# Kernel tuning notes

Hardware: AMD Instinct MI355X
Metric: run time of the kernel (lower is better)

## Reference

```python
import jax, jax.numpy as jnp
import numpy as np

D_MODEL = 256
N_LAYERS = 4
D_STATE = 16
D_CONV = 4
EXPAND = 2
HEADDIM = 64
D_INNER = EXPAND * D_MODEL            # 512
NHEADS = D_INNER // HEADDIM           # 8
CONV_DIM = D_INNER + 2 * D_STATE      # 544 (ngroups=1)
D_IN_PROJ = 2 * D_INNER + 2 * D_STATE + NHEADS  # 1064
VOCAB = 8
MAXLEN = 2048
NCLASSES = 2
PAD_IDX = 4
EPS = 1e-5
B, L = 8, 2048


def setup_inputs() -> dict:
    key = jax.random.key(0)
    ks = jax.random.split(key, 10)
    x = jax.random.randint(ks[0], (B, L), 0, VOCAB)
    attention_mask = jnp.ones((B, L), jnp.float32)
    embedding = 0.02 * jax.random.normal(ks[1], (VOCAB, D_MODEL), jnp.float32)
    embedding = embedding.at[PAD_IDX].set(0.0)  # padding_idx row is zero
    pos_embedding = 0.02 * jax.random.normal(ks[2], (1, MAXLEN, D_MODEL), jnp.float32)
    in_proj_w = 0.05 * jax.random.normal(ks[3], (N_LAYERS, D_IN_PROJ, D_MODEL), jnp.float32)
    conv_w = 0.3 * jax.random.normal(ks[4], (N_LAYERS, CONV_DIM, D_CONV), jnp.float32)
    conv_b = jnp.zeros((N_LAYERS, CONV_DIM), jnp.float32)
    # dt_bias = softplus^{-1}(dt) with dt ~ U(0.001, 0.1), as in mamba_ssm init
    dt = jax.random.uniform(ks[5], (N_LAYERS, NHEADS), jnp.float32, 0.001, 0.1)
    dt_bias = jnp.log(jnp.expm1(dt))
    A_log = jnp.log(jax.random.uniform(ks[6], (N_LAYERS, NHEADS), jnp.float32, 1.0, 16.0))
    D_param = jnp.ones((N_LAYERS, NHEADS), jnp.float32)
    norm_w = jnp.ones((N_LAYERS, D_INNER), jnp.float32)
    out_proj_w = 0.05 * jax.random.normal(ks[7], (N_LAYERS, D_MODEL, D_INNER), jnp.float32)
    ln_w = jnp.ones((D_MODEL,), jnp.float32)
    ln_b = jnp.zeros((D_MODEL,), jnp.float32)
    cls_w = 0.05 * jax.random.normal(ks[8], (NCLASSES, D_MODEL), jnp.float32)
    cls_b = jnp.zeros((NCLASSES,), jnp.float32)
    return dict(x=x, attention_mask=attention_mask, embedding=embedding,
                pos_embedding=pos_embedding, in_proj_w=in_proj_w, conv_w=conv_w,
                conv_b=conv_b, dt_bias=dt_bias, A_log=A_log, D_param=D_param,
                norm_w=norm_w, out_proj_w=out_proj_w, ln_w=ln_w, ln_b=ln_b,
                cls_w=cls_w, cls_b=cls_b)


def _mamba2(h_in, Wi, cw, cb, dtb, Alog, Dp, nw, Wo):
    """One Mamba2 block (ngroups=1, headdim=64, norm_before_gate=False)."""
    b, l, _ = h_in.shape
    zxbcdt = jnp.einsum('bld,ed->ble', h_in, Wi)          # (b,l,1064)
    z = zxbcdt[..., :D_INNER]                             # gate
    xBC = zxbcdt[..., D_INNER:D_INNER + CONV_DIM]
    dt = jax.nn.softplus(zxbcdt[..., D_INNER + CONV_DIM:] + dtb)  # (b,l,h)
    # causal depthwise conv1d (kernel D_CONV) + silu
    xp = jnp.pad(xBC, ((0, 0), (D_CONV - 1, 0), (0, 0)))
    xwin = jnp.stack([xp[:, k:k + l, :] for k in range(D_CONV)], axis=-1)  # (b,l,c,k)
    xBC = jax.nn.silu(jnp.einsum('blck,ck->blc', xwin, cw) + cb)
    xs = xBC[..., :D_INNER].reshape(b, l, NHEADS, HEADDIM)
    Bm = xBC[..., D_INNER:D_INNER + D_STATE]              # (b,l,n)
    Cm = xBC[..., D_INNER + D_STATE:]                     # (b,l,n)
    dA = jnp.exp(dt * (-jnp.exp(Alog)))                   # (b,l,h)
    dtx = dt[..., None] * xs                              # (b,l,h,p)

    def step(h, inp):
        dA_t, dtx_t, B_t, C_t = inp
        h = dA_t[:, :, None, None] * h + dtx_t[..., None] * B_t[:, None, None, :]
        y = jnp.einsum('bhpn,bn->bhp', h, C_t)
        return h, y

    h0 = jnp.zeros((b, NHEADS, HEADDIM, D_STATE), h_in.dtype)
    _, ys = jax.lax.scan(step, h0, (jnp.swapaxes(dA, 0, 1), jnp.swapaxes(dtx, 0, 1),
                                    jnp.swapaxes(Bm, 0, 1), jnp.swapaxes(Cm, 0, 1)))
    y = jnp.swapaxes(ys, 0, 1) + Dp[None, None, :, None] * xs  # skip term D*x
    y = y.reshape(b, l, D_INNER) * jax.nn.silu(z)               # gate, then RMSNorm
    y = y * jax.lax.rsqrt(jnp.mean(jnp.square(y), axis=-1, keepdims=True) + EPS) * nw
    return jnp.einsum('ble,de->bld', y, Wo)


def _layer_norm(h, w, b):
    mu = jnp.mean(h, -1, keepdims=True)
    var = jnp.mean(jnp.square(h - mu), -1, keepdims=True)
    return (h - mu) * jax.lax.rsqrt(var + EPS) * w + b


def reference(x, attention_mask, embedding, pos_embedding, in_proj_w, conv_w,
              conv_b, dt_bias, A_log, D_param, norm_w, out_proj_w, ln_w, ln_b,
              cls_w, cls_b):
    l = x.shape[1]
    h = embedding[x] + pos_embedding[:, :l, :]
    m = attention_mask[..., None]
    h = h * m
    for i in range(N_LAYERS):
        res = h
        h = _mamba2(h, in_proj_w[i], conv_w[i], conv_b[i], dt_bias[i],
                    A_log[i], D_param[i], norm_w[i], out_proj_w[i])
        h = _layer_norm(h + res, ln_w, ln_b)
        h = h * m
    pooled = jnp.mean(h, axis=1)   # dropout is identity at eval
    return pooled @ cls_w.T + cls_b
```

## Files before the change

### kernel.cpp

```cpp
#include <hip/hip_runtime.h>
#include <hip/hip_bf16.h>
#include <math.h>

#define B_ 8
#define L_ 2048
#define DM 256
#define DIP 1064
#define DI 512
#define CD 544
#define DSZ 16
#define NH 8
#define HD 64
#define Q_ 64
#define NC 32

typedef __attribute__((ext_vector_type(8))) short bf16x8;
typedef __attribute__((ext_vector_type(4))) float f32x4;

__device__ inline unsigned short f2bf(float f) {
    __hip_bfloat16 h = __float2bfloat16(f);
    return *(unsigned short*)&h;
}
__device__ inline float bf2f(unsigned short u) {
    unsigned int x = ((unsigned int)u) << 16;
    return __uint_as_float(x);
}
__device__ inline float fast_sig(float x) {
    return __builtin_amdgcn_rcpf(1.f + __expf(-x));
}

__global__ __launch_bounds__(256) void k_f2bf(const float* __restrict__ in, unsigned short* __restrict__ out, int n4) {
    int i = blockIdx.x * 256 + threadIdx.x;
    if (i >= n4) return;
    float4 v = *(const float4*)(in + (size_t)i * 4);
    ushort4 o;
    o.x = f2bf(v.x); o.y = f2bf(v.y); o.z = f2bf(v.z); o.w = f2bf(v.w);
    *(ushort4*)(out + (size_t)i * 4) = o;
}

__global__ __launch_bounds__(256) void k_embed(const int* __restrict__ x, const float* __restrict__ mask,
                                               const float* __restrict__ emb, const float* __restrict__ pos,
                                               float* __restrict__ h, unsigned short* __restrict__ h_bf) {
    int i = blockIdx.x * 256 + threadIdx.x;
    if (i >= B_ * L_ * DM) return;
    int d = i % DM;
    int bl = i / DM;
    int l = bl % L_;
    int tok = x[bl];
    float v = (emb[tok * DM + d] + pos[l * DM + d]) * mask[bl];
    h[i] = v;
    h_bf[i] = f2bf(v);
}

template <int OUTMODE>
__global__ __launch_bounds__(256) void k_gemm(const unsigned short* __restrict__ A, int lda,
                                              const unsigned short* __restrict__ Bw, int ldb, int N,
                                              void* __restrict__ Cout, int ldc, int K,
                                              float* __restrict__ dtraw) {
    __shared__ unsigned short Al[2][128 * 32];
    __shared__ unsigned short Bl[2][128 * 32];
    int tid = threadIdx.x;
    int l = tid & 63;
    int w = tid >> 6, wr = w >> 1, wc = w & 1;
    int m0 = blockIdx.x * 128, n0 = blockIdx.y * 128;

    f32x4 zero = {0.f, 0.f, 0.f, 0.f};
    f32x4 acc[4][4];
#pragma unroll
    for (int i = 0; i < 4; i++)
#pragma unroll
        for (int j = 0; j < 4; j++) acc[i][j] = zero;

    int lr = l & 15, kq = l >> 4;
    int aoff = (wr * 64 + lr) * 32 + kq * 8;
    int boff = (wc * 64 + lr) * 32 + kq * 8;

    auto stage = [&](int ks, int buf) {
        int k0 = ks * 32;
#pragma unroll
        for (int q = 0; q < 2; q++) {
            int c = tid + q * 256;
            int row = c >> 2, cc = (c & 3) * 8;
            const unsigned short* ga = A + (size_t)(m0 + row) * lda + k0 + cc;
            __builtin_amdgcn_global_load_lds((const __attribute__((address_space(1))) void*)ga,
                                             (__attribute__((address_space(3))) void*)(&Al[buf][c * 8]), 16, 0, 0);
            int rowb = n0 + row;
            if (rowb > N - 1) rowb = N - 1;
            const unsigned short* gb = Bw + (size_t)rowb * ldb + k0 + cc;
            __builtin_amdgcn_global_load_lds((const __attribute__((address_space(1))) void*)gb,
                                             (__attribute__((address_space(3))) void*)(&Bl[buf][c * 8]), 16, 0, 0);
        }
    };

    stage(0, 0);
    int ksteps = K / 32;
    for (int s = 0; s < ksteps; s++) {
        int buf = s & 1;
        __syncthreads();
        if (s + 1 < ksteps) stage(s + 1, buf ^ 1);
        bf16x8 a[4], b[4];
#pragma unroll
        for (int i = 0; i < 4; i++) a[i] = *(const bf16x8*)&Al[buf][aoff + i * 512];
#pragma unroll
        for (int j = 0; j < 4; j++) b[j] = *(const bf16x8*)&Bl[buf][boff + j * 512];
#pragma unroll
        for (int i = 0; i < 4; i++)
#pragma unroll
            for (int j = 0; j < 4; j++)
                acc[i][j] = __builtin_amdgcn_mfma_f32_16x16x32_bf16(a[i], b[j], acc[i][j], 0, 0, 0);
    }

#pragma unroll
    for (int i = 0; i < 4; i++) {
        int m = m0 + wr * 64 + i * 16 + kq * 4;
#pragma unroll
        for (int j = 0; j < 4; j++) {
            int n = n0 + wc * 64 + j * 16 + lr;
            if (n < N) {
                if (OUTMODE == 0) {
                    float* C = (float*)Cout;
#pragma unroll
                    for (int r = 0; r < 4; r++)
                        C[(size_t)(m + r) * ldc + n] = acc[i][j][r];
                } else {
                    unsigned short* C = (unsigned short*)Cout;
#pragma unroll
                    for (int r = 0; r < 4; r++)
                        C[(size_t)(m + r) * ldc + n] = f2bf(acc[i][j][r]);
                    if (OUTMODE == 1 && n >= DI + CD) {
#pragma unroll
                        for (int r = 0; r < 4; r++)
                            dtraw[(size_t)(m + r) * NH + (n - (DI + CD))] = acc[i][j][r];
                    }
                }
            }
        }
    }
}

__global__ __launch_bounds__(256) void k_scan1c(const unsigned short* __restrict__ zxb,
                                                const float* __restrict__ dtraw,
                                                const float* __restrict__ cw, const float* __restrict__ cb,
                                                const float* __restrict__ dtb, const float* __restrict__ Alog,
                                                const float* __restrict__ Dp,
                                                unsigned short* __restrict__ ybuf, float* __restrict__ Sg,
                                                float* __restrict__ Pg, float* __restrict__ cumLg,
                                                float* __restrict__ Cc) {
    int bh = blockIdx.x, c = blockIdx.y;
    int b = bh >> 3, h = bh & 7;
    int tid = threadIdx.x;
    int t0 = c * Q_;
    int w = tid >> 6, l = tid & 63;
    int lr = l & 15, kq = l >> 4;

    __shared__ __align__(16) unsigned short Zl[67 * 96];
    __shared__ __align__(16) unsigned short Xt[Q_ * 72];
    __shared__ __align__(16) unsigned short Cbf[Q_ * 32];
    __shared__ __align__(16) unsigned short Bbf[Q_ * 32];
    __shared__ __align__(16) unsigned short Btw[DSZ * 72];
    __shared__ float Lc[Q_], dts[Q_], coefS[Q_];
    unsigned short* Mbf = Zl;

    float Dval = Dp[h];

    for (int idx = tid; idx < 67 * 12; idx += 256) {
        int rr = idx / 12, seg = idx - rr * 12;
        int lg = t0 - 3 + rr;
        bf16x8 v;
        if (lg >= 0) {
            const unsigned short* src = zxb + (size_t)(b * L_ + lg) * DIP +
                                        (seg < 8 ? (DI + h * HD + seg * 8) : (1024 + (seg - 8) * 8));
            v = *(const bf16x8*)src;
        } else {
#pragma unroll
            for (int j = 0; j < 8; j++) v[j] = 0;
        }
        int col = (seg < 8) ? seg * 8 : (64 + (seg - 8) * 8);
        *(bf16x8*)&Zl[rr * 96 + col] = v;
    }
    {
        bf16x8 z8;
#pragma unroll
        for (int j = 0; j < 8; j++) z8[j] = 0;
        *(bf16x8*)&Cbf[tid * 8] = z8;
        *(bf16x8*)&Bbf[tid * 8] = z8;
    }
    if (tid < 64) {
        float raw = dtraw[(size_t)(b * L_ + t0 + tid) * NH + h] + dtb[h];
        float dtv = (raw > 20.f) ? raw : log1pf(__expf(raw));
        float v = -__expf(Alog[h]) * dtv;
#pragma unroll
        for (int off = 1; off < 64; off <<= 1) {
            float u = __shfl_up(v, off);
            if (tid >= off) v += u;
        }
        dts[tid] = dtv;
        Lc[tid] = v;
        float lend = __shfl(v, 63);
        coefS[tid] = __expf(lend - v) * dtv;
        cumLg[(size_t)(bh * NC + c) * Q_ + tid] = v;
        if (tid == 63) Pg[bh * NC + c] = __expf(v);
    }
    __syncthreads();

    float xreg[4][4];
#pragma unroll
    for (int pt = 0; pt < 4; pt++) {
#pragma unroll
        for (int r = 0; r < 4; r++) {
            int t = w * 16 + kq * 4 + r;
            int p = pt * 16 + lr;
            int cc = h * HD + p;
            float acc = cb[cc];
#pragma unroll
            for (int k = 0; k < 4; k++)
                acc = fmaf(bf2f(Zl[(t + k) * 96 + p]), cw[cc * 4 + k], acc);
            float s = acc * fast_sig(acc);
            xreg[pt][r] = s;
            Xt[p * 72 + t] = f2bf(s);
        }
    }
    for (int idx = tid; idx < Q_ * 32; idx += 256) {
        int t = idx >> 5, n32 = idx & 31;
        int cc = DI + n32;
        float acc = cb[cc];
#pragma unroll
        for (int k = 0; k < 4; k++)
            acc = fmaf(bf2f(Zl[(t + k) * 96 + 64 + n32]), cw[cc * 4 + k], acc);
        float s = acc * fast_sig(acc);
        if (n32 < 16) {
            int n = n32;
            Bbf[t * 32 + (((n >> 3) ^ (t & 3)) * 8) + (n & 7)] = f2bf(dts[t] * s);
            Btw[n * 72 + t] = f2bf(coefS[t] * s);
        } else {
            int n = n32 - 16;
            Cbf[t * 32 + (((n >> 3) ^ (t & 3)) * 8) + (n & 7)] = f2bf(s);
            if (h == 0) Cc[((size_t)(b * L_ + t0 + t)) * DSZ + n] = s;
        }
    }
    __syncthreads();

    f32x4 zero = {0.f, 0.f, 0.f, 0.f};

    f32x4 cbt[4];
    {
        bf16x8 af = *(const bf16x8*)&Cbf[(w * 16 + lr) * 32 + ((kq ^ (lr & 3)) * 8)];
#pragma unroll
        for (int st = 0; st < 4; st++) {
            bf16x8 bf = *(const bf16x8*)&Bbf[(st * 16 + lr) * 32 + ((kq ^ (lr & 3)) * 8)];
            cbt[st] = __builtin_amdgcn_mfma_f32_16x16x32_bf16(af, bf, zero, 0, 0, 0);
        }
    }
#pragma unroll
    for (int st = 0; st < 4; st++) {
#pragma unroll
        for (int r = 0; r < 4; r++) {
            int t = w * 16 + kq * 4 + r;
            int s = st * 16 + lr;
            float m = (s <= t) ? __expf(Lc[t] - Lc[s]) * cbt[st][r] : 0.f;
            Mbf[t * 64 + (((s >> 3) ^ (t & 7)) * 8) + (s & 7)] = f2bf(m);
        }
    }
    __syncthreads();

    {
        unsigned short* base_y = ybuf + ((size_t)b * L_ + t0) * DI + h * HD;
        f32x4 acc[4];
#pragma unroll
        for (int pt = 0; pt < 4; pt++) acc[pt] = zero;
#pragma unroll
        for (int ks = 0; ks < 2; ks++) {
            bf16x8 af = *(const bf16x8*)&Mbf[(w * 16 + lr) * 64 + (((ks * 4 + kq) ^ (lr & 7)) * 8)];
#pragma unroll
            for (int pt = 0; pt < 4; pt++) {
                bf16x8 bf = *(const bf16x8*)&Xt[(pt * 16 + lr) * 72 + ks * 32 + kq * 8];
                acc[pt] = __builtin_amdgcn_mfma_f32_16x16x32_bf16(af, bf, acc[pt], 0, 0, 0);
            }
        }
#pragma unroll
        for (int pt = 0; pt < 4; pt++) {
#pragma unroll
            for (int r = 0; r < 4; r++) {
                int t = w * 16 + kq * 4 + r;
                int p = pt * 16 + lr;
                base_y[(size_t)t * DI + p] = f2bf(acc[pt][r] + Dval * xreg[pt][r]);
            }
        }
    }

    {
        f32x4 sacc = zero;
#pragma unroll
        for (int ks = 0; ks < 2; ks++) {
            bf16x8 af = *(const bf16x8*)&Xt[(w * 16 + lr) * 72 + ks * 32 + kq * 8];
            bf16x8 bf = *(const bf16x8*)&Btw[lr * 72 + ks * 32 + kq * 8];
            sacc = __builtin_amdgcn_mfma_f32_16x16x32_bf16(af, bf, sacc, 0, 0, 0);
        }
#pragma unroll
        for (int r = 0; r < 4; r++) {
            int p = w * 16 + kq * 4 + r;
            Sg[((size_t)(bh * NC + c) * HD + p) * DSZ + lr] = sacc[r];
        }
    }
}

__global__ __launch_bounds__(256) void k_scan2(const float* __restrict__ Sg, const float* __restrict__ Pg,
                                               float* __restrict__ Hg) {
    int bh = blockIdx.x;
    int tid = threadIdx.x;
    int p = tid >> 2, n0 = (tid & 3) * 4;
    float4 H = make_float4(0.f, 0.f, 0.f, 0.f);
    for (int g = 0; g < NC / 8; g++) {
        float4 S[8];
#pragma unroll
        for (int j = 0; j < 8; j++)
            S[j] = *(const float4*)(Sg + (((size_t)bh * NC + g * 8 + j) * HD + p) * DSZ + n0);
#pragma unroll
        for (int j = 0; j < 8; j++) {
            int cc = g * 8 + j;
            *(float4*)(Hg + (((size_t)bh * NC + cc) * HD + p) * DSZ + n0) = H;
            float P = Pg[bh * NC + cc];
            H.x = fmaf(P, H.x, S[j].x);
            H.y = fmaf(P, H.y, S[j].y);
            H.z = fmaf(P, H.z, S[j].z);
            H.w = fmaf(P, H.w, S[j].w);
        }
    }
}

__global__ __launch_bounds__(256) void k_scan3g(const unsigned short* __restrict__ ybuf,
                                                const unsigned short* __restrict__ zxb,
                                                const float* __restrict__ Hg, const float* __restrict__ cumLg,
                                                const float* __restrict__ Cc, const float* __restrict__ nw,
                                                unsigned short* __restrict__ yn_bf) {
    int b = blockIdx.x, by = blockIdx.y;
    int c64 = by >> 2, tl0 = (by & 3) * 16;
    int t0 = by * 16;
    int tid = threadIdx.x;
    __shared__ float Hsn[DSZ * 576];
    __shared__ float Lq[NH][16];

    {
        int p = tid & 63, hp = tid >> 6;
#pragma unroll
        for (int ho = 0; ho < 2; ho++) {
            int hh = hp * 2 + ho;
            const float* src = Hg + (((size_t)(b * NH + hh) * NC + c64) * HD + p) * DSZ;
            float* dst = &Hsn[p * 9 + hh];
#pragma unroll
            for (int nq = 0; nq < 4; nq++) {
                float4 v = *(const float4*)(src + nq * 4);
                dst[(nq * 4 + 0) * 576] = v.x;
                dst[(nq * 4 + 1) * 576] = v.y;
                dst[(nq * 4 + 2) * 576] = v.z;
                dst[(nq * 4 + 3) * 576] = v.w;
            }
        }
    }
    if (tid < 128) {
        int hh = tid >> 4, t = tid & 15;
        Lq[hh][t] = cumLg[((size_t)(b * NH + hh) * NC + c64) * Q_ + tl0 + t];
    }
    __syncthreads();

    int t = tid >> 4, q = tid & 15;
    int hh = q >> 1, p0 = (q & 1) * 32;
    size_t bl = (size_t)b * L_ + t0 + t;
    float ef = __expf(Lq[hh][t]);

    float Cr[16];
#pragma unroll
    for (int k = 0; k < 4; k++) {
        float4 v = *(const float4*)(Cc + bl * DSZ + k * 4);
        Cr[4 * k + 0] = ef * v.x;
        Cr[4 * k + 1] = ef * v.y;
        Cr[4 * k + 2] = ef * v.z;
        Cr[4 * k + 3] = ef * v.w;
    }

    const unsigned short* yrow = ybuf + bl * DI + hh * HD + p0;
    const unsigned short* zrow = zxb + bl * DIP + hh * HD + p0;
    unsigned short yv[32], zv[32];
#pragma unroll
    for (int k = 0; k < 4; k++) *(bf16x8*)&yv[k * 8] = *(const bf16x8*)(yrow + k * 8);
#pragma unroll
    for (int k = 0; k < 4; k++) *(bf16x8*)&zv[k * 8] = *(const bf16x8*)(zrow + k * 8);

    float yg[32];
    float ss = 0.f;
#pragma unroll
    for (int j = 0; j < 32; j++) {
        const float* hp_ = &Hsn[(p0 + j) * 9 + hh];
        float d = 0.f;
#pragma unroll
        for (int n = 0; n < DSZ; n++) d = fmaf(Cr[n], hp_[n * 576], d);
        float y = bf2f(yv[j]) + d;
        float z = bf2f(zv[j]);
        yg[j] = y * z * fast_sig(z);
        ss = fmaf(yg[j], yg[j], ss);
    }
    ss += __shfl_xor(ss, 1);
    ss += __shfl_xor(ss, 2);
    ss += __shfl_xor(ss, 4);
    ss += __shfl_xor(ss, 8);
    float r = rsqrtf(ss * (1.f / DI) + 1e-5f);

    const float* nwp = nw + hh * HD + p0;
    unsigned short* dst = yn_bf + bl * DI + hh * HD + p0;
#pragma unroll
    for (int k = 0; k < 4; k++) {
        bf16x8 o;
#pragma unroll
        for (int j = 0; j < 8; j++) o[j] = (short)f2bf(yg[k * 8 + j] * r * nwp[k * 8 + j]);
        *(bf16x8*)(dst + k * 8) = o;
    }
}

__global__ __launch_bounds__(256) void k_ln(const unsigned short* __restrict__ tmp, float* __restrict__ h,
                                            unsigned short* __restrict__ h_bf,
                                            const float* __restrict__ lnw, const float* __restrict__ lnb,
                                            const float* __restrict__ mask) {
    int row = blockIdx.x * 4 + (threadIdx.x >> 6);
    int lane = threadIdx.x & 63;
    size_t base = (size_t)row * DM + lane * 4;
    ushort4 tv = *(const ushort4*)(tmp + base);
    float4 hv = *(const float4*)(h + base);
    float v[4] = {bf2f(tv.x) + hv.x, bf2f(tv.y) + hv.y, bf2f(tv.z) + hv.z, bf2f(tv.w) + hv.w};
    float s = v[0] + v[1] + v[2] + v[3];
#pragma unroll
    for (int m = 1; m < 64; m <<= 1) s += __shfl_xor(s, m);
    float mu = s * (1.f / DM);
    float q = 0.f;
#pragma unroll
    for (int j = 0; j < 4; j++) {
        float d = v[j] - mu;
        q = fmaf(d, d, q);
    }
#pragma unroll
    for (int m = 1; m < 64; m <<= 1) q += __shfl_xor(q, m);
    float rs = rsqrtf(q * (1.f / DM) + 1e-5f);
    float mk = mask[row];
    float4 wv = *(const float4*)(lnw + lane * 4);
    float4 bv = *(const float4*)(lnb + lane * 4);
    float o[4];
    o[0] = ((v[0] - mu) * rs * wv.x + bv.x) * mk;
    o[1] = ((v[1] - mu) * rs * wv.y + bv.y) * mk;
    o[2] = ((v[2] - mu) * rs * wv.z + bv.z) * mk;
    o[3] = ((v[3] - mu) * rs * wv.w + bv.w) * mk;
    *(float4*)(h + base) = make_float4(o[0], o[1], o[2], o[3]);
    ushort4 ob;
    ob.x = f2bf(o[0]); ob.y = f2bf(o[1]); ob.z = f2bf(o[2]); ob.w = f2bf(o[3]);
    *(ushort4*)(h_bf + base) = ob;
}

__global__ __launch_bounds__(256) void k_pool1(const float* __restrict__ h, float* __restrict__ part) {
    int b = blockIdx.x, g = blockIdx.y, d = threadIdx.x;
    const float* hb = h + ((size_t)b * L_ + g * 128) * DM + d;
    float s = 0.f;
    for (int l = 0; l < 128; l++) s += hb[(size_t)l * DM];
    part[((size_t)b * 16 + g) * DM + d] = s;
}

__global__ __launch_bounds__(256) void k_pool2(const float* __restrict__ part, const float* __restrict__ cw,
                                               const float* __restrict__ cb, float* __restrict__ out) {
    int b = blockIdx.x, tid = threadIdx.x;
    float s = 0.f;
#pragma unroll
    for (int g = 0; g < 16; g++) s += part[((size_t)b * 16 + g) * DM + tid];
    s *= (1.0f / L_);
    float p0 = s * cw[tid];
    float p1 = s * cw[DM + tid];
#pragma unroll
    for (int m = 1; m < 64; m <<= 1) {
        p0 += __shfl_xor(p0, m);
        p1 += __shfl_xor(p1, m);
    }
    __shared__ float r0[4], r1[4];
    if ((tid & 63) == 0) { r0[tid >> 6] = p0; r1[tid >> 6] = p1; }
    __syncthreads();
    if (tid == 0) {
        out[b * 2 + 0] = r0[0] + r0[1] + r0[2] + r0[3] + cb[0];
        out[b * 2 + 1] = r1[0] + r1[1] + r1[2] + r1[3] + cb[1];
    }
}

extern "C" void kernel_launch(void* const* d_in, const int* in_sizes, int n_in,
                              void* d_out, int out_size, void* d_ws, size_t ws_size,
                              hipStream_t stream) {
    const int*   x    = (const int*)d_in[0];
    const float* mask = (const float*)d_in[1];
    const float* emb  = (const float*)d_in[2];
    const float* pos  = (const float*)d_in[3];
    const float* Wi   = (const float*)d_in[4];
    const float* cw   = (const float*)d_in[5];
    const float* cb   = (const float*)d_in[6];
    const float* dtb  = (const float*)d_in[7];
    const float* Alog = (const float*)d_in[8];
    const float* Dp   = (const float*)d_in[9];
    const float* nw   = (const float*)d_in[10];
    const float* Wo   = (const float*)d_in[11];
    const float* lnw  = (const float*)d_in[12];
    const float* lnb  = (const float*)d_in[13];
    const float* clsw = (const float*)d_in[14];
    const float* clsb = (const float*)d_in[15];
    float* out = (float*)d_out;

    float* ws    = (float*)d_ws;
    float* h     = ws;
    float* dtraw = h + (size_t)B_ * L_ * DM;
    float* Sg    = dtraw + (size_t)B_ * L_ * NH;
    float* Pg    = Sg + (size_t)64 * NC * HD * DSZ;
    float* cumL  = Pg + (size_t)64 * NC;
    float* Hg    = cumL + (size_t)64 * NC * Q_;
    float* Cc    = Hg + (size_t)64 * NC * HD * DSZ;
    float* pool  = Cc + (size_t)B_ * L_ * DSZ;
    unsigned short* zxb   = (unsigned short*)(pool + (size_t)B_ * 16 * DM);
    unsigned short* ybuf  = zxb + (size_t)B_ * L_ * DIP;
    unsigned short* tmp   = ybuf + (size_t)B_ * L_ * DI;
    unsigned short* h_bf  = tmp + (size_t)B_ * L_ * DM;
    unsigned short* yn_bf = h_bf + (size_t)B_ * L_ * DM;
    unsigned short* Wi_bf = yn_bf + (size_t)B_ * L_ * DI;
    unsigned short* Wo_bf = Wi_bf + (size_t)4 * DIP * DM;

    k_f2bf<<<(4 * DIP * DM / 4 + 255) / 256, 256, 0, stream>>>(Wi, Wi_bf, 4 * DIP * DM / 4);
    k_f2bf<<<(4 * DM * DI / 4 + 255) / 256, 256, 0, stream>>>(Wo, Wo_bf, 4 * DM * DI / 4);

    k_embed<<<(B_ * L_ * DM + 255) / 256, 256, 0, stream>>>(x, mask, emb, pos, h, h_bf);

    for (int i = 0; i < 4; i++) {
        k_gemm<1><<<dim3(B_ * L_ / 128, (DIP + 127) / 128), 256, 0, stream>>>(
            h_bf, DM, Wi_bf + (size_t)i * DIP * DM, DM, DIP, zxb, DIP, DM, dtraw);
        k_scan1c<<<dim3(64, NC), 256, 0, stream>>>(
            zxb, dtraw, cw + (size_t)i * CD * 4, cb + i * CD, dtb + i * NH, Alog + i * NH,
            Dp + i * NH, ybuf, Sg, Pg, cumL, Cc);
        k_scan2<<<64, 256, 0, stream>>>(Sg, Pg, Hg);
        k_scan3g<<<dim3(B_, 128), 256, 0, stream>>>(ybuf, zxb, Hg, cumL, Cc, nw + (size_t)i * DI, yn_bf);
        k_gemm<2><<<dim3(B_ * L_ / 128, DM / 128), 256, 0, stream>>>(
            yn_bf, DI, Wo_bf + (size_t)i * DM * DI, DI, DM, tmp, DM, DI, nullptr);
        k_ln<<<B_ * L_ / 4, 256, 0, stream>>>(tmp, h, h_bf, lnw, lnb, mask);
    }

    k_pool1<<<dim3(B_, 16), 256, 0, stream>>>(h, pool);
    k_pool2<<<B_, 256, 0, stream>>>(pool, clsw, clsb, out);
}
```

Baseline: 416.7 us.

## Fuse out-projection GEMM with residual add and LayerNorm, drop fp32 hidden state

Replaces the out-projection GEMM plus separate LayerNorm kernel with a single kernel that computes 32-row by 256-column tiles, adds the residual read from the bf16 hidden state, and does the row LayerNorm in-register with cross-wave reductions through shared memory. The fp32 hidden-state buffer and the intermediate tmp buffer are removed, and pooling now reads bf16. This cuts a kernel launch and several full-tensor round trips through memory. In exchange the residual stream is held only in bf16, which loses precision across layers, and variance is computed as E[x^2]-mu^2 in a single pass.

```diff
diff --git a/kernel.cpp b/kernel.cpp
--- a/kernel.cpp
+++ b/kernel.cpp
@@ -40,7 +40,7 @@
 
 __global__ __launch_bounds__(256) void k_embed(const int* __restrict__ x, const float* __restrict__ mask,
                                                const float* __restrict__ emb, const float* __restrict__ pos,
-                                               float* __restrict__ h, unsigned short* __restrict__ h_bf) {
+                                               unsigned short* __restrict__ h_bf) {
     int i = blockIdx.x * 256 + threadIdx.x;
     if (i >= B_ * L_ * DM) return;
     int d = i % DM;
@@ -48,7 +48,6 @@
     int l = bl % L_;
     int tok = x[bl];
     float v = (emb[tok * DM + d] + pos[l * DM + d]) * mask[bl];
-    h[i] = v;
     h_bf[i] = f2bf(v);
 }
 
@@ -117,22 +116,130 @@
         for (int j = 0; j < 4; j++) {
             int n = n0 + wc * 64 + j * 16 + lr;
             if (n < N) {
-                if (OUTMODE == 0) {
-                    float* C = (float*)Cout;
+                unsigned short* C = (unsigned short*)Cout;
+#pragma unroll
+                for (int r = 0; r < 4; r++)
+                    C[(size_t)(m + r) * ldc + n] = f2bf(acc[i][j][r]);
+                if (OUTMODE == 1 && n >= DI + CD) {
 #pragma unroll
                     for (int r = 0; r < 4; r++)
-                        C[(size_t)(m + r) * ldc + n] = acc[i][j][r];
-                } else {
-                    unsigned short* C = (unsigned short*)Cout;
-#pragma unroll
-                    for (int r = 0; r < 4; r++)
-                        C[(size_t)(m + r) * ldc + n] = f2bf(acc[i][j][r]);
-                    if (OUTMODE == 1 && n >= DI + CD) {
-#pragma unroll
-                        for (int r = 0; r < 4; r++)
-                            dtraw[(size_t)(m + r) * NH + (n - (DI + CD))] = acc[i][j][r];
-                    }
+                        dtraw[(size_t)(m + r) * NH + (n - (DI + CD))] = acc[i][j][r];
                 }
+            }
+        }
+    }
+}
+
+__global__ __launch_bounds__(256) void k_gemm_ln(const unsigned short* __restrict__ A,
+                                                 const unsigned short* __restrict__ Bw,
+                                                 unsigned short* __restrict__ hbf,
+                                                 const float* __restrict__ lnw, const float* __restrict__ lnb,
+                                                 const float* __restrict__ mask) {
+    __shared__ unsigned short Al[2][32 * 32];
+    __shared__ unsigned short Bl[2][256 * 32];
+    __shared__ float part_s[32][4], part_q[32][4];
+    int tid = threadIdx.x;
+    int l = tid & 63;
+    int w = tid >> 6;
+    int m0 = blockIdx.x * 32;
+    int lr = l & 15, kq = l >> 4;
+
+    f32x4 zero = {0.f, 0.f, 0.f, 0.f};
+    f32x4 acc[2][4];
+#pragma unroll
+    for (int i = 0; i < 2; i++)
+#pragma unroll
+        for (int j = 0; j < 4; j++) acc[i][j] = zero;
+
+    auto stage = [&](int ks, int buf) {
+        int k0 = ks * 32;
+        if (tid < 128) {
+            int row = tid >> 2, cc = (tid & 3) * 8;
+            const unsigned short* ga = A + (size_t)(m0 + row) * DI + k0 + cc;
+            __builtin_amdgcn_global_load_lds((const __attribute__((address_space(1))) void*)ga,
+                                             (__attribute__((address_space(3))) void*)(&Al[buf][tid * 8]), 16, 0, 0);
+        }
+#pragma unroll
+        for (int q = 0; q < 4; q++) {
+            int c = tid + q * 256;
+            int row = c >> 2, cc = (c & 3) * 8;
+            const unsigned short* gb = Bw + (size_t)row * DI + k0 + cc;
+            __builtin_amdgcn_global_load_lds((const __attribute__((address_space(1))) void*)gb,
+                                             (__attribute__((address_space(3))) void*)(&Bl[buf][c * 8]), 16, 0, 0);
+        }
+    };
+
+    stage(0, 0);
+    const int ksteps = DI / 32;
+    for (int s = 0; s < ksteps; s++) {
+        int buf = s & 1;
+        __syncthreads();
+        if (s + 1 < ksteps) stage(s + 1, buf ^ 1);
+        bf16x8 a[2], b[4];
+#pragma unroll
+        for (int i = 0; i < 2; i++) a[i] = *(const bf16x8*)&Al[buf][(i * 16 + lr) * 32 + kq * 8];
+#pragma unroll
+        for (int j = 0; j < 4; j++) b[j] = *(const bf16x8*)&Bl[buf][(w * 64 + j * 16 + lr) * 32 + kq * 8];
+#pragma unroll
+        for (int i = 0; i < 2; i++)
+#pragma unroll
+            for (int j = 0; j < 4; j++)
+                acc[i][j] = __builtin_amdgcn_mfma_f32_16x16x32_bf16(a[i], b[j], acc[i][j], 0, 0, 0);
+    }
+
+#pragma unroll
+    for (int i = 0; i < 2; i++) {
+#pragma unroll
+        for (int r = 0; r < 4; r++) {
+            int row = i * 16 + kq * 4 + r;
+            const unsigned short* hrow = hbf + (size_t)(m0 + row) * DM + w * 64 + lr;
+#pragma unroll
+            for (int j = 0; j < 4; j++)
+                acc[i][j][r] += bf2f(hrow[j * 16]);
+        }
+    }
+#pragma unroll
+    for (int i = 0; i < 2; i++) {
+#pragma unroll
+        for (int r = 0; r < 4; r++) {
+            float sv = acc[i][0][r] + acc[i][1][r] + acc[i][2][r] + acc[i][3][r];
+            float qv = acc[i][0][r] * acc[i][0][r] + acc[i][1][r] * acc[i][1][r] +
+                       acc[i][2][r] * acc[i][2][r] + acc[i][3][r] * acc[i][3][r];
+#pragma unroll
+            for (int off = 1; off < 16; off <<= 1) {
+                sv += __shfl_xor(sv, off);
+                qv += __shfl_xor(qv, off);
+            }
+            if (lr == 0) {
+                int row = i * 16 + kq * 4 + r;
+                part_s[row][w] = sv;
+                part_q[row][w] = qv;
+            }
+        }
+    }
+    __syncthreads();
+    float4 wv4 = make_float4(lnw[w * 64 + 0 * 16 + lr], lnw[w * 64 + 1 * 16 + lr],
+                             lnw[w * 64 + 2 * 16 + lr], lnw[w * 64 + 3 * 16 + lr]);
+    float4 bv4 = make_float4(lnb[w * 64 + 0 * 16 + lr], lnb[w * 64 + 1 * 16 + lr],
+                             lnb[w * 64 + 2 * 16 + lr], lnb[w * 64 + 3 * 16 + lr]);
+#pragma unroll
+    for (int i = 0; i < 2; i++) {
+#pragma unroll
+        for (int r = 0; r < 4; r++) {
+            int row = i * 16 + kq * 4 + r;
+            float sum = part_s[row][0] + part_s[row][1] + part_s[row][2] + part_s[row][3];
+            float sq  = part_q[row][0] + part_q[row][1] + part_q[row][2] + part_q[row][3];
+            float mu = sum * (1.f / DM);
+            float var = sq * (1.f / DM) - mu * mu;
+            float rs = rsqrtf(var + 1e-5f);
+            float mk = mask[m0 + row];
+            unsigned short* drow = hbf + (size_t)(m0 + row) * DM + w * 64 + lr;
+            float wr_[4] = {wv4.x, wv4.y, wv4.z, wv4.w};
+            float br_[4] = {bv4.x, bv4.y, bv4.z, bv4.w};
+#pragma unroll
+            for (int j = 0; j < 4; j++) {
+                float o = ((acc[i][j][r] - mu) * rs * wr_[j] + br_[j]) * mk;
+                drow[j * 16] = f2bf(o);
             }
         }
     }
@@ -416,48 +523,11 @@
     }
 }
 
-__global__ __launch_bounds__(256) void k_ln(const unsigned short* __restrict__ tmp, float* __restrict__ h,
-                                            unsigned short* __restrict__ h_bf,
-                                            const float* __restrict__ lnw, const float* __restrict__ lnb,
-                                            const float* __restrict__ mask) {
-    int row = blockIdx.x * 4 + (threadIdx.x >> 6);
-    int lane = threadIdx.x & 63;
-    size_t base = (size_t)row * DM + lane * 4;
-    ushort4 tv = *(const ushort4*)(tmp + base);
-    float4 hv = *(const float4*)(h + base);
-    float v[4] = {bf2f(tv.x) + hv.x, bf2f(tv.y) + hv.y, bf2f(tv.z) + hv.z, bf2f(tv.w) + hv.w};
-    float s = v[0] + v[1] + v[2] + v[3];
-#pragma unroll
-    for (int m = 1; m < 64; m <<= 1) s += __shfl_xor(s, m);
-    float mu = s * (1.f / DM);
-    float q = 0.f;
-#pragma unroll
-    for (int j = 0; j < 4; j++) {
-        float d = v[j] - mu;
-        q = fmaf(d, d, q);
-    }
-#pragma unroll
-    for (int m = 1; m < 64; m <<= 1) q += __shfl_xor(q, m);
-    float rs = rsqrtf(q * (1.f / DM) + 1e-5f);
-    float mk = mask[row];
-    float4 wv = *(const float4*)(lnw + lane * 4);
-    float4 bv = *(const float4*)(lnb + lane * 4);
-    float o[4];
-    o[0] = ((v[0] - mu) * rs * wv.x + bv.x) * mk;
-    o[1] = ((v[1] - mu) * rs * wv.y + bv.y) * mk;
-    o[2] = ((v[2] - mu) * rs * wv.z + bv.z) * mk;
-    o[3] = ((v[3] - mu) * rs * wv.w + bv.w) * mk;
-    *(float4*)(h + base) = make_float4(o[0], o[1], o[2], o[3]);
-    ushort4 ob;
-    ob.x = f2bf(o[0]); ob.y = f2bf(o[1]); ob.z = f2bf(o[2]); ob.w = f2bf(o[3]);
-    *(ushort4*)(h_bf + base) = ob;
-}
-
-__global__ __launch_bounds__(256) void k_pool1(const float* __restrict__ h, float* __restrict__ part) {
+__global__ __launch_bounds__(256) void k_pool1(const unsigned short* __restrict__ h, float* __restrict__ part) {
     int b = blockIdx.x, g = blockIdx.y, d = threadIdx.x;
-    const float* hb = h + ((size_t)b * L_ + g * 128) * DM + d;
+    const unsigned short* hb = h + ((size_t)b * L_ + g * 128) * DM + d;
     float s = 0.f;
-    for (int l = 0; l < 128; l++) s += hb[(size_t)l * DM];
+    for (int l = 0; l < 128; l++) s += bf2f(hb[(size_t)l * DM]);
     part[((size_t)b * 16 + g) * DM + d] = s;
 }
 
@@ -506,8 +576,7 @@
     float* out = (float*)d_out;
 
     float* ws    = (float*)d_ws;
-    float* h     = ws;
-    float* dtraw = h + (size_t)B_ * L_ * DM;
+    float* dtraw = ws;
     float* Sg    = dtraw + (size_t)B_ * L_ * NH;
     float* Pg    = Sg + (size_t)64 * NC * HD * DSZ;
     float* cumL  = Pg + (size_t)64 * NC;
@@ -516,8 +585,7 @@
     float* pool  = Cc + (size_t)B_ * L_ * DSZ;
     unsigned short* zxb   = (unsigned short*)(pool + (size_t)B_ * 16 * DM);
     unsigned short* ybuf  = zxb + (size_t)B_ * L_ * DIP;
-    unsigned short* tmp   = ybuf + (size_t)B_ * L_ * DI;
-    unsigned short* h_bf  = tmp + (size_t)B_ * L_ * DM;
+    unsigned short* h_bf  = ybuf + (size_t)B_ * L_ * DI;
     unsigned short* yn_bf = h_bf + (size_t)B_ * L_ * DM;
     unsigned short* Wi_bf = yn_bf + (size_t)B_ * L_ * DI;
     unsigned short* Wo_bf = Wi_bf + (size_t)4 * DIP * DM;
@@ -525,7 +593,7 @@
     k_f2bf<<<(4 * DIP * DM / 4 + 255) / 256, 256, 0, stream>>>(Wi, Wi_bf, 4 * DIP * DM / 4);
     k_f2bf<<<(4 * DM * DI / 4 + 255) / 256, 256, 0, stream>>>(Wo, Wo_bf, 4 * DM * DI / 4);
 
-    k_embed<<<(B_ * L_ * DM + 255) / 256, 256, 0, stream>>>(x, mask, emb, pos, h, h_bf);
+    k_embed<<<(B_ * L_ * DM + 255) / 256, 256, 0, stream>>>(x, mask, emb, pos, h_bf);
 
     for (int i = 0; i < 4; i++) {
         k_gemm<1><<<dim3(B_ * L_ / 128, (DIP + 127) / 128), 256, 0, stream>>>(
@@ -535,11 +603,10 @@
             Dp + i * NH, ybuf, Sg, Pg, cumL, Cc);
         k_scan2<<<64, 256, 0, stream>>>(Sg, Pg, Hg);
         k_scan3g<<<dim3(B_, 128), 256, 0, stream>>>(ybuf, zxb, Hg, cumL, Cc, nw + (size_t)i * DI, yn_bf);
-        k_gemm<2><<<dim3(B_ * L_ / 128, DM / 128), 256, 0, stream>>>(
-            yn_bf, DI, Wo_bf + (size_t)i * DM * DI, DI, DM, tmp, DM, DI, nullptr);
-        k_ln<<<B_ * L_ / 4, 256, 0, stream>>>(tmp, h, h_bf, lnw, lnb, mask);
-    }
-
-    k_pool1<<<dim3(B_, 16), 256, 0, stream>>>(h, pool);
+        k_gemm_ln<<<B_ * L_ / 32, 256, 0, stream>>>(
+            yn_bf, Wo_bf + (size_t)i * DM * DI, h_bf, lnw, lnb, mask);
+    }
+
+    k_pool1<<<dim3(B_, 16), 256, 0, stream>>>(h_bf, pool);
     k_pool2<<<B_, 256, 0, stream>>>(pool, clsw, clsb, out);
 }
```

After: 384.1 us. -7.8%, faster.
